# Optimization experiments

Measured on AMD Instinct MI355X. Metric: run time of the kernel, lower is better.

The kernel has to match this reference:

```python
import jax, jax.numpy as jnp
import numpy as np

B, S, D = 4, 2048, 2048
H = 16
Q_LORA = 1536
KV_LORA = 512
D_NOPE = 128
D_ROPE = 64
D_V = 128
MLP = 8192
EPS = 1e-6
THETA = 10000.0


def rmsnorm(x, scale, eps=EPS):
    var = jnp.mean(jnp.square(x.astype(jnp.float32)), axis=-1, keepdims=True)
    return (x * jax.lax.rsqrt(var + eps)).astype(x.dtype) * scale


def rope(x, positions):
    # x: [B, S, H, d], positions: [B, S]
    d = x.shape[-1]
    inv_freq = 1.0 / (THETA ** (jnp.arange(0, d, 2, dtype=jnp.float32) / d))
    ang = positions.astype(jnp.float32)[..., None] * inv_freq  # [B,S,d/2]
    cos = jnp.cos(ang)[:, :, None, :]
    sin = jnp.sin(ang)[:, :, None, :]
    x1, x2 = jnp.split(x, 2, axis=-1)
    return jnp.concatenate([x1 * cos - x2 * sin, x2 * cos + x1 * sin], axis=-1)


def setup_inputs() -> dict:
    key = jax.random.key(0)
    ks = jax.random.split(key, 16)
    sd = lambda fan: 1.0 / np.sqrt(fan)
    inp = {
        'inputs': jax.random.normal(ks[0], (B, S, D), jnp.float32),
        'decoder_segment_ids': jnp.ones((B, S), jnp.int32),
        'decoder_positions': jnp.broadcast_to(jnp.arange(S, dtype=jnp.int32), (B, S)),
        'pre_ln_scale': jnp.ones((D,), jnp.float32),
        'post_ln_scale': jnp.ones((D,), jnp.float32),
        'q_ln_scale': jnp.ones((Q_LORA,), jnp.float32),
        'kv_ln_scale': jnp.ones((KV_LORA,), jnp.float32),
        'wq_a': jax.random.normal(ks[1], (D, Q_LORA), jnp.float32) * sd(D),
        'wq_b': jax.random.normal(ks[2], (Q_LORA, H, D_NOPE + D_ROPE), jnp.float32) * sd(Q_LORA),
        'wkv_a': jax.random.normal(ks[3], (D, KV_LORA + D_ROPE), jnp.float32) * sd(D),
        'wkv_b': jax.random.normal(ks[4], (KV_LORA, H, D_NOPE + D_V), jnp.float32) * sd(KV_LORA),
        'wo_attn': jax.random.normal(ks[5], (H, D_V, D), jnp.float32) * sd(H * D_V),
        'wi_0': jax.random.normal(ks[6], (D, MLP), jnp.float32) * sd(D),
        'wi_1': jax.random.normal(ks[7], (D, MLP), jnp.float32) * sd(D),
        'wo_mlp': jax.random.normal(ks[8], (MLP, D), jnp.float32) * sd(MLP),
    }
    return inp


def reference(inputs, decoder_segment_ids, decoder_positions, pre_ln_scale, post_ln_scale,
              q_ln_scale, kv_ln_scale, wq_a, wq_b, wkv_a, wkv_b, wo_attn, wi_0, wi_1, wo_mlp):
    # ---- pre-norm ----
    lnx = rmsnorm(inputs, pre_ln_scale)

    # ---- MLA attention ----
    # low-rank query: down-proj, norm, up-proj
    q_c = rmsnorm(lnx @ wq_a, q_ln_scale)                       # [B,S,Q_LORA]
    q = jnp.einsum('bsr,rhd->bshd', q_c, wq_b)                  # [B,S,H,nope+rope]
    q_nope, q_rope = q[..., :D_NOPE], q[..., D_NOPE:]

    # compressed kv + decoupled rope key
    kv = lnx @ wkv_a                                            # [B,S,KV_LORA+rope]
    c_kv = rmsnorm(kv[..., :KV_LORA], kv_ln_scale)
    k_rope = kv[..., KV_LORA:][:, :, None, :]                   # [B,S,1,rope]
    kvu = jnp.einsum('bsr,rhd->bshd', c_kv, wkv_b)              # [B,S,H,nope+v]
    k_nope, v = kvu[..., :D_NOPE], kvu[..., D_NOPE:]

    q_rope = rope(q_rope, decoder_positions)
    k_rope = rope(k_rope, decoder_positions)
    k_rope = jnp.broadcast_to(k_rope, (B, S, H, D_ROPE))

    qf = jnp.concatenate([q_nope, q_rope], axis=-1)             # [B,S,H,192]
    kf = jnp.concatenate([k_nope, k_rope], axis=-1)

    scale = 1.0 / np.sqrt(D_NOPE + D_ROPE)
    scores = jnp.einsum('bqhd,bkhd->bhqk', qf, kf) * scale      # [B,H,S,S]

    pos = decoder_positions
    seg = decoder_segment_ids
    mask = (pos[:, :, None] >= pos[:, None, :]) & (seg[:, :, None] == seg[:, None, :])
    scores = jnp.where(mask[:, None, :, :], scores, -1e9)
    probs = jax.nn.softmax(scores, axis=-1)

    attn = jnp.einsum('bhqk,bkhd->bqhd', probs, v)              # [B,S,H,D_V]
    attn_out = jnp.einsum('bqhd,hdm->bqm', attn, wo_attn)       # [B,S,D]

    # ---- residual + post-norm ----
    intermediate = inputs + attn_out
    hidden = rmsnorm(intermediate, post_ln_scale)

    # ---- gated MLP (silu * linear) ----
    mlp = (jax.nn.silu(hidden @ wi_0) * (hidden @ wi_1)) @ wo_mlp

    return mlp + intermediate
```

## Files before the change

kernel.cpp:

```cpp
#include <hip/hip_runtime.h>
#include <stdint.h>

typedef unsigned short u16;
typedef __bf16 bf16x8 __attribute__((ext_vector_type(8)));
typedef float f32x4 __attribute__((ext_vector_type(4)));

#define B_ 4
#define S_ 2048
#define H_ 16
#define TOK (B_*S_)
#define MFMA_B16 __builtin_amdgcn_mfma_f32_16x16x32_bf16

__device__ __forceinline__ u16 f32_bf16(float f) {
    union { float f; unsigned int u; } x; x.f = f;
    return (u16)((x.u + 0x7fffu + ((x.u >> 16) & 1u)) >> 16);
}
__device__ __forceinline__ float bf2f(u16 v) {
    union { unsigned int u; float f; } x; x.u = ((unsigned int)v) << 16; return x.f;
}
__device__ __forceinline__ void gld_lds16(const u16* g, u16* lds) {
    __builtin_amdgcn_global_load_lds(
        (const __attribute__((address_space(1))) unsigned int*)g,
        (__attribute__((address_space(3))) unsigned int*)lds, 16, 0, 0);
}

__global__ void fill_sentinel(float* o, int n) {
    int i = blockIdx.x * 256 + threadIdx.x;
    if (i < n) o[i] = 12345.0f;
}

__global__ __launch_bounds__(256) void transpose_f32_bf16(const float* __restrict__ in, u16* __restrict__ out,
                                                          int K, int N, int Npad) {
    __shared__ float t[32][33];
    int nb = blockIdx.x * 32, kb = blockIdx.y * 32;
    int c = threadIdx.x & 31, r = threadIdx.x >> 5;
#pragma unroll
    for (int i = 0; i < 4; ++i) {
        int kk = kb + r + i * 8, nn = nb + c;
        t[r + i * 8][c] = (kk < K && nn < N) ? in[(size_t)kk * N + nn] : 0.f;
    }
    __syncthreads();
#pragma unroll
    for (int i = 0; i < 4; ++i) {
        int no = nb + r + i * 8, ko = kb + c;
        if (no < Npad && ko < K) out[(size_t)no * K + ko] = f32_bf16(t[c][r + i * 8]);
    }
}

__global__ __launch_bounds__(256) void rmsnorm_f32(const float* __restrict__ in, const float* __restrict__ sc,
                                                   u16* __restrict__ out, int N) {
    int row = blockIdx.x;
    const float* x = in + (size_t)row * N;
    float ss = 0.f;
    for (int c = threadIdx.x * 4; c < N; c += 1024) {
        float4 v = *(const float4*)(x + c);
        ss += v.x * v.x + v.y * v.y + v.z * v.z + v.w * v.w;
    }
#pragma unroll
    for (int off = 32; off; off >>= 1) ss += __shfl_down(ss, off);
    __shared__ float red[4];
    if ((threadIdx.x & 63) == 0) red[threadIdx.x >> 6] = ss;
    __syncthreads();
    float rs = rsqrtf((red[0] + red[1] + red[2] + red[3]) / (float)N + 1e-6f);
    for (int c = threadIdx.x * 4; c < N; c += 1024) {
        float4 v = *(const float4*)(x + c);
        float4 s4 = *(const float4*)(sc + c);
        ushort4 ov;
        ov.x = f32_bf16(v.x * rs * s4.x);
        ov.y = f32_bf16(v.y * rs * s4.y);
        ov.z = f32_bf16(v.z * rs * s4.z);
        ov.w = f32_bf16(v.w * rs * s4.w);
        *(ushort4*)&out[(size_t)row * N + c] = ov;
    }
}

__global__ __launch_bounds__(256) void rmsnorm_bf16(const u16* __restrict__ in, const float* __restrict__ sc,
                                                    u16* __restrict__ out, int N) {
    int row = blockIdx.x;
    const u16* x = in + (size_t)row * N;
    float ss = 0.f;
    for (int c = threadIdx.x * 8; c < N; c += 2048) {
        ushort4 v0 = *(const ushort4*)(x + c);
        ushort4 v1 = *(const ushort4*)(x + c + 4);
        float f0 = bf2f(v0.x), f1 = bf2f(v0.y), f2 = bf2f(v0.z), f3 = bf2f(v0.w);
        float f4 = bf2f(v1.x), f5 = bf2f(v1.y), f6 = bf2f(v1.z), f7 = bf2f(v1.w);
        ss += f0*f0 + f1*f1 + f2*f2 + f3*f3 + f4*f4 + f5*f5 + f6*f6 + f7*f7;
    }
#pragma unroll
    for (int off = 32; off; off >>= 1) ss += __shfl_down(ss, off);
    __shared__ float red[4];
    if ((threadIdx.x & 63) == 0) red[threadIdx.x >> 6] = ss;
    __syncthreads();
    float rs = rsqrtf((red[0] + red[1] + red[2] + red[3]) / (float)N + 1e-6f);
    for (int c = threadIdx.x * 8; c < N; c += 2048) {
        ushort4 v0 = *(const ushort4*)(x + c);
        ushort4 v1 = *(const ushort4*)(x + c + 4);
        ushort4 o0, o1;
        o0.x = f32_bf16(bf2f(v0.x) * rs * sc[c + 0]);
        o0.y = f32_bf16(bf2f(v0.y) * rs * sc[c + 1]);
        o0.z = f32_bf16(bf2f(v0.z) * rs * sc[c + 2]);
        o0.w = f32_bf16(bf2f(v0.w) * rs * sc[c + 3]);
        o1.x = f32_bf16(bf2f(v1.x) * rs * sc[c + 4]);
        o1.y = f32_bf16(bf2f(v1.y) * rs * sc[c + 5]);
        o1.z = f32_bf16(bf2f(v1.z) * rs * sc[c + 6]);
        o1.w = f32_bf16(bf2f(v1.w) * rs * sc[c + 7]);
        *(ushort4*)&out[(size_t)row * N + c] = o0;
        *(ushort4*)&out[(size_t)row * N + c + 4] = o1;
    }
}

__global__ __launch_bounds__(128) void kv_post(const u16* __restrict__ kv, const float* __restrict__ scale,
                                               const int* __restrict__ pos, u16* __restrict__ ckv,
                                               u16* __restrict__ kr) {
    int row = blockIdx.x;
    const u16* x = kv + (size_t)row * 640;
    int c = threadIdx.x * 4;
    ushort4 v = *(const ushort4*)(x + c);
    float f0 = bf2f(v.x), f1 = bf2f(v.y), f2 = bf2f(v.z), f3 = bf2f(v.w);
    float ss = f0*f0 + f1*f1 + f2*f2 + f3*f3;
#pragma unroll
    for (int off = 32; off; off >>= 1) ss += __shfl_down(ss, off);
    __shared__ float red[2];
    if ((threadIdx.x & 63) == 0) red[threadIdx.x >> 6] = ss;
    __syncthreads();
    float rs = rsqrtf((red[0] + red[1]) * (1.f / 512.f) + 1e-6f);
    float4 s4 = *(const float4*)(scale + c);
    ushort4 ov;
    ov.x = f32_bf16(f0 * rs * s4.x);
    ov.y = f32_bf16(f1 * rs * s4.y);
    ov.z = f32_bf16(f2 * rs * s4.z);
    ov.w = f32_bf16(f3 * rs * s4.w);
    *(ushort4*)&ckv[(size_t)row * 512 + c] = ov;
    if (threadIdx.x < 32) {
        int i = threadIdx.x;
        float x1 = bf2f(x[512 + i]), x2 = bf2f(x[544 + i]);
        float inv = expf(-(float)(2 * i) * (1.f / 64.f) * 9.2103403719761836f);
        float ang = (float)pos[row] * inv;
        float sn, cs; sincosf(ang, &sn, &cs);
        kr[(size_t)row * 64 + i]      = f32_bf16(x1 * cs - x2 * sn);
        kr[(size_t)row * 64 + 32 + i] = f32_bf16(x2 * cs + x1 * sn);
    }
}

__global__ __launch_bounds__(64) void q_rope_inplace(u16* __restrict__ q, const int* __restrict__ pos) {
    int token = blockIdx.x, h = blockIdx.y;
    u16* p = q + ((size_t)token * 16 + h) * 192;
    int t = threadIdx.x, i = t & 31;
    float x1 = bf2f(p[128 + i]), x2 = bf2f(p[160 + i]);
    float inv = expf(-(float)(2 * i) * (1.f / 64.f) * 9.2103403719761836f);
    float ang = (float)pos[token] * inv;
    float sn, cs; sincosf(ang, &sn, &cs);
    float val = (t < 32) ? (x1 * cs - x2 * sn) : (x2 * cs + x1 * sn);
    p[128 + t] = f32_bf16(val);
}

__global__ __launch_bounds__(320) void kv_build(const u16* __restrict__ kvu, const u16* __restrict__ kr,
                                                u16* __restrict__ kf, u16* __restrict__ vf, int tok0) {
    int local = blockIdx.x, h = blockIdx.y;
    int token = tok0 + local;
    int b = token >> 11, s = token & 2047;
    int bh = b * 16 + h;
    int tile = s >> 6, ki = s & 63;
    const u16* u = kvu + ((size_t)local * 16 + h) * 256;
    int t = threadIdx.x;
    if (t < 192) {
        u16 val = (t < 128) ? u[t] : kr[(size_t)token * 64 + (t - 128)];
        int byte = (ki * 384 + t * 2) ^ ((ki & 7) << 4);
        kf[(size_t)bh * (S_ * 192) + (size_t)tile * 12288 + (byte >> 1)] = val;
    } else {
        int dv = t - 192;
        u16 val = u[128 + dv];
        int byte = (dv * 128 + ki * 2) ^ ((dv & 7) << 4);
        vf[(size_t)bh * (S_ * 128) + (size_t)tile * 8192 + (byte >> 1)] = val;
    }
}

__global__ __launch_bounds__(256) void gemm128(const u16* __restrict__ A, const u16* __restrict__ Bt,
                                               u16* __restrict__ C, int M, int N, int K) {
    __shared__ u16 As[128 * 32];
    __shared__ u16 Bs[128 * 32];
    const int l = threadIdx.x & 63, w = threadIdx.x >> 6;
    const int wr = w >> 1, wc = w & 1;
    const int m0 = blockIdx.y * 128, n0 = blockIdx.x * 128;
    const int lm = l & 15, lg = l >> 4;
    const int srow = l >> 2, sk = (l & 3) * 8;
    f32x4 acc[4][4] = {};
    for (int k0 = 0; k0 < K; k0 += 32) {
#pragma unroll
        for (int i = 0; i < 2; ++i) {
            int c = w * 2 + i;
            gld_lds16(A  + (size_t)(m0 + c * 16 + srow) * K + k0 + sk, &As[c * 512]);
            gld_lds16(Bt + (size_t)(n0 + c * 16 + srow) * K + k0 + sk, &Bs[c * 512]);
        }
        __syncthreads();
        bf16x8 a[4], b[4];
#pragma unroll
        for (int m = 0; m < 4; ++m) a[m] = *(const bf16x8*)&As[(wr * 64 + m * 16 + lm) * 32 + lg * 8];
#pragma unroll
        for (int n = 0; n < 4; ++n) b[n] = *(const bf16x8*)&Bs[(wc * 64 + n * 16 + lm) * 32 + lg * 8];
#pragma unroll
        for (int m = 0; m < 4; ++m)
#pragma unroll
            for (int n = 0; n < 4; ++n)
                acc[m][n] = MFMA_B16(a[m], b[n], acc[m][n], 0, 0, 0);
        __syncthreads();
    }
#pragma unroll
    for (int m = 0; m < 4; ++m)
#pragma unroll
        for (int j = 0; j < 4; ++j) {
            int row = m0 + wr * 64 + m * 16 + lg * 4 + j;
            size_t base = (size_t)row * N + n0 + wc * 64;
#pragma unroll
            for (int n = 0; n < 4; ++n)
                C[base + n * 16 + lm] = f32_bf16(acc[m][n][j]);
        }
}

template<int EPI>
__global__ __launch_bounds__(512, 2) void gemm256(const u16* __restrict__ A, const u16* __restrict__ Bt,
                                                  void* __restrict__ Cv, const void* __restrict__ Rv,
                                                  int M, int N, int K) {
    __shared__ u16 lds[65536];
    char* ldsb = (char*)lds;
    const int tid = threadIdx.x;
    const int l = tid & 63, w = tid >> 6;
    const int wr = w >> 2, wcn = w & 3;
    const int lm = l & 15, lg = l >> 4;
    const int m0 = blockIdx.y * 256, n0 = blockIdx.x * 256;

    int srow[2], scb[2];
#pragma unroll
    for (int ld = 0; ld < 2; ++ld) {
        int P = tid * 16 + ld * 8192;
        int L = P ^ (((P >> 7) & 7) << 4);
        srow[ld] = L >> 7; scb[ld] = L & 127;
    }
    const u16* Ablk = A + (size_t)m0 * K;
    const u16* Bblk = Bt + (size_t)n0 * K;

    f32x4 acc[8][4] = {};

    auto stage = [&](const u16* gp, int h, int kt, int db, int streamoff) {
#pragma unroll
        for (int ld = 0; ld < 2; ++ld) {
            const u16* src = gp + (size_t)(h * 128 + srow[ld]) * K + kt * 64 + (scb[ld] >> 1);
            u16* dst = (u16*)(ldsb + db * 65536 + streamoff + h * 16384 + w * 1024 + ld * 8192);
            gld_lds16(src, dst);
        }
    };
    auto readA = [&](int db, int fm, int ks) -> bf16x8 {
        int row = wr * 128 + fm * 16 + lm;
        int cb = lg * 16 + ks * 64;
        return *(const bf16x8*)(ldsb + db * 65536 + row * 128 + (cb ^ ((row & 7) << 4)));
    };
    auto readB = [&](int db, int fn, int ks) -> bf16x8 {
        int row = wcn * 64 + fn * 16 + lm;
        int cb = lg * 16 + ks * 64;
        return *(const bf16x8*)(ldsb + db * 65536 + 32768 + row * 128 + (cb ^ ((row & 7) << 4)));
    };

    const int ntile = K >> 6;
#pragma unroll
    for (int h = 0; h < 2; ++h) stage(Ablk, h, 0, 0, 0);
#pragma unroll
    for (int h = 0; h < 2; ++h) stage(Bblk, h, 0, 0, 32768);
    asm volatile("s_waitcnt vmcnt(0)" ::: "memory");
    __builtin_amdgcn_s_barrier();

    for (int t = 0; t < ntile; ++t) {
        const int db = t & 1;
        bf16x8 bfr[4][2];
        bf16x8 a0 = readA(db, 0, 0), a1 = readA(db, 0, 1);
        bf16x8 a2 = readA(db, 1, 0), a3 = readA(db, 1, 1);
#pragma unroll
        for (int fn = 0; fn < 4; ++fn) { bfr[fn][0] = readB(db, fn, 0); bfr[fn][1] = readB(db, fn, 1); }
        if (t + 1 < ntile) {
#pragma unroll
            for (int h = 0; h < 2; ++h) stage(Ablk, h, t + 1, db ^ 1, 0);
#pragma unroll
            for (int h = 0; h < 2; ++h) stage(Bblk, h, t + 1, db ^ 1, 32768);
        }
        __builtin_amdgcn_s_barrier();
        asm volatile("s_waitcnt lgkmcnt(0)" ::: "memory");
        __builtin_amdgcn_sched_barrier(0);
        __builtin_amdgcn_s_setprio(1);
#pragma unroll
        for (int fn = 0; fn < 4; ++fn) {
            acc[0][fn] = MFMA_B16(a0, bfr[fn][0], acc[0][fn], 0, 0, 0);
            acc[0][fn] = MFMA_B16(a1, bfr[fn][1], acc[0][fn], 0, 0, 0);
            acc[1][fn] = MFMA_B16(a2, bfr[fn][0], acc[1][fn], 0, 0, 0);
            acc[1][fn] = MFMA_B16(a3, bfr[fn][1], acc[1][fn], 0, 0, 0);
        }
        __builtin_amdgcn_s_setprio(0);
        __builtin_amdgcn_s_barrier();
#pragma unroll
        for (int p = 1; p < 4; ++p) {
            a0 = readA(db, 2 * p, 0);     a1 = readA(db, 2 * p, 1);
            a2 = readA(db, 2 * p + 1, 0); a3 = readA(db, 2 * p + 1, 1);
            if (p == 3) asm volatile("s_waitcnt vmcnt(0)" ::: "memory");
            __builtin_amdgcn_s_barrier();
            asm volatile("s_waitcnt lgkmcnt(0)" ::: "memory");
            __builtin_amdgcn_sched_barrier(0);
            __builtin_amdgcn_s_setprio(1);
#pragma unroll
            for (int fn = 0; fn < 4; ++fn) {
                acc[2*p][fn]   = MFMA_B16(a0, bfr[fn][0], acc[2*p][fn], 0, 0, 0);
                acc[2*p][fn]   = MFMA_B16(a1, bfr[fn][1], acc[2*p][fn], 0, 0, 0);
                acc[2*p+1][fn] = MFMA_B16(a2, bfr[fn][0], acc[2*p+1][fn], 0, 0, 0);
                acc[2*p+1][fn] = MFMA_B16(a3, bfr[fn][1], acc[2*p+1][fn], 0, 0, 0);
            }
            __builtin_amdgcn_s_setprio(0);
            __builtin_amdgcn_s_barrier();
        }
    }
#pragma unroll
    for (int fm = 0; fm < 8; ++fm)
#pragma unroll
        for (int j = 0; j < 4; ++j) {
            int row = m0 + wr * 128 + fm * 16 + lg * 4 + j;
            size_t base = (size_t)row * N + n0 + wcn * 64;
#pragma unroll
            for (int fn = 0; fn < 4; ++fn) {
                size_t idx = base + fn * 16 + lm;
                float v = acc[fm][fn][j];
                if (EPI == 0) {
                    ((u16*)Cv)[idx] = f32_bf16(v);
                } else if (EPI == 1) {
                    ((float*)Cv)[idx] = v + ((const float*)Rv)[idx];
                } else {
                    float x0 = bf2f(((const u16*)Rv)[idx]);
                    float sl = x0 / (1.f + expf(-x0));
                    ((u16*)Cv)[idx] = f32_bf16(sl * v);
                }
            }
        }
}

__global__ __launch_bounds__(256) void attn_fwd(const u16* __restrict__ qf, const u16* __restrict__ kfs,
                                                const u16* __restrict__ vfs, u16* __restrict__ attn) {
    __shared__ u16 Ks[64 * 192];
    __shared__ u16 Vs[128 * 64];
    __shared__ u16 Ps[4][1024];
    const int px = blockIdx.x;
    const int bh = blockIdx.y;
    const int b = bh >> 4, h = bh & 15;
    const int l = threadIdx.x & 63, w = threadIdx.x >> 6;
    const int lm = l & 15, g = l >> 4;
    const u16* kb0 = kfs + (size_t)bh * (S_ * 192);
    const u16* vb0 = vfs + (size_t)bh * (S_ * 128);
    const float scale = 0.07216878364870322f;

    for (int pass = 0; pass < 2; ++pass) {
        const int qb = pass ? (31 - px) : px;
        const int qrow = qb * 64 + w * 16 + lm;
        const u16* qp = qf + (((size_t)(b * S_ + qrow)) * 16 + h) * 192 + g * 8;
        bf16x8 qr[6];
#pragma unroll
        for (int c = 0; c < 6; ++c) qr[c] = *(const bf16x8*)(qp + c * 32);
        f32x4 o[8] = {};
        float mrow[4] = {-1e30f, -1e30f, -1e30f, -1e30f};
        float lrow[4] = {0.f, 0.f, 0.f, 0.f};
        for (int kt = 0; kt <= qb; ++kt) {
            const u16* kc = kb0 + (size_t)kt * 12288;
            const u16* vc = vb0 + (size_t)kt * 8192;
#pragma unroll
            for (int i = 0; i < 6; ++i) {
                int c = w + i * 4;
                gld_lds16(kc + c * 512 + l * 8, &Ks[c * 512]);
            }
#pragma unroll
            for (int i = 0; i < 4; ++i) {
                int c = w + i * 4;
                gld_lds16(vc + c * 512 + l * 8, &Vs[c * 512]);
            }
            __syncthreads();
            f32x4 sc[4] = {};
#pragma unroll
            for (int nf = 0; nf < 4; ++nf) {
                int key = nf * 16 + lm;
                int kswz = (key & 7) << 4;
#pragma unroll
                for (int c = 0; c < 6; ++c) {
                    int byte = (key * 384 + (c * 32 + g * 8) * 2) ^ kswz;
                    bf16x8 kv = *(const bf16x8*)((const char*)Ks + byte);
                    sc[nf] = MFMA_B16(qr[c], kv, sc[nf], 0, 0, 0);
                }
            }
#pragma unroll
            for (int j = 0; j < 4; ++j) {
                const int q_g = qb * 64 + w * 16 + g * 4 + j;
                float mx = -1e30f;
#pragma unroll
                for (int nf = 0; nf < 4; ++nf) {
                    int key_g = kt * 64 + nf * 16 + lm;
                    float v = sc[nf][j] * scale;
                    v = (key_g > q_g) ? -1e30f : v;
                    sc[nf][j] = v;
                    mx = fmaxf(mx, v);
                }
                mx = fmaxf(mx, __shfl_xor(mx, 1));
                mx = fmaxf(mx, __shfl_xor(mx, 2));
                mx = fmaxf(mx, __shfl_xor(mx, 4));
                mx = fmaxf(mx, __shfl_xor(mx, 8));
                float newm = fmaxf(mrow[j], mx);
                float fac = __expf(mrow[j] - newm);
                mrow[j] = newm;
                float rs = 0.f;
                u16 pb[4];
#pragma unroll
                for (int nf = 0; nf < 4; ++nf) {
                    float pv = __expf(sc[nf][j] - newm);
                    rs += pv;
                    pb[nf] = f32_bf16(pv);
                }
                rs += __shfl_xor(rs, 1);
                rs += __shfl_xor(rs, 2);
                rs += __shfl_xor(rs, 4);
                rs += __shfl_xor(rs, 8);
                lrow[j] = lrow[j] * fac + rs;
#pragma unroll
                for (int n = 0; n < 8; ++n) o[n][j] *= fac;
                int row = g * 4 + j;
                int rswz = (row & 7) << 4;
#pragma unroll
                for (int nf = 0; nf < 4; ++nf) {
                    int byte = (row * 128 + (nf * 16 + lm) * 2) ^ rswz;
                    *(u16*)((char*)&Ps[w][0] + byte) = pb[nf];
                }
            }
#pragma unroll
            for (int kc2 = 0; kc2 < 2; ++kc2) {
                int pbyte = (lm * 128 + (kc2 * 32 + g * 8) * 2) ^ ((lm & 7) << 4);
                bf16x8 pa = *(const bf16x8*)((const char*)&Ps[w][0] + pbyte);
#pragma unroll
                for (int n = 0; n < 8; ++n) {
                    int dv = n * 16 + lm;
                    int vbyte = (dv * 128 + (kc2 * 32 + g * 8) * 2) ^ ((dv & 7) << 4);
                    bf16x8 vv = *(const bf16x8*)((const char*)Vs + vbyte);
                    o[n] = MFMA_B16(pa, vv, o[n], 0, 0, 0);
                }
            }
            __syncthreads();
        }
#pragma unroll
        for (int j = 0; j < 4; ++j) {
            float inv = 1.f / lrow[j];
            int s = qb * 64 + w * 16 + g * 4 + j;
            size_t base = ((size_t)(b * S_ + s)) * (H_ * 128) + h * 128;
#pragma unroll
            for (int n = 0; n < 8; ++n)
                attn[base + n * 16 + lm] = f32_bf16(o[n][j] * inv);
        }
    }
}

extern "C" void kernel_launch(void* const* d_in, const int* in_sizes, int n_in,
                              void* d_out, int out_size, void* d_ws, size_t ws_size,
                              hipStream_t stream) {
    (void)in_sizes; (void)n_in;
    const float* inputs = (const float*)d_in[0];
    const int*   pos    = (const int*)d_in[2];
    const float* pre_s  = (const float*)d_in[3];
    const float* post_s = (const float*)d_in[4];
    const float* q_s    = (const float*)d_in[5];
    const float* kv_s   = (const float*)d_in[6];
    const float* wq_a   = (const float*)d_in[7];
    const float* wq_b   = (const float*)d_in[8];
    const float* wkv_a  = (const float*)d_in[9];
    const float* wkv_b  = (const float*)d_in[10];
    const float* wo_at  = (const float*)d_in[11];
    const float* wi0    = (const float*)d_in[12];
    const float* wi1    = (const float*)d_in[13];
    const float* wom    = (const float*)d_in[14];
    float* out = (float*)d_out;

    char* p = (char*)d_ws;
    auto alloc = [&](size_t n) { char* r = p; p += (n + 255) & ~(size_t)255; return r; };
    char* R1   = alloc((size_t)134217728);
    u16* vf    = (u16*)alloc((size_t)33554432);
    u16* aslot = (u16*)alloc((size_t)33554432);
    u16* wslot = (u16*)alloc((size_t)33554432);
    u16* ckv   = (u16*)alloc((size_t)8388608);
    u16* krope = (u16*)alloc((size_t)1048576);
    if ((size_t)(p - (char*)d_ws) > ws_size) {
        fill_sentinel<<<(out_size + 255) / 256, 256, 0, stream>>>(out, out_size);
        return;
    }
    u16* kf    = (u16*)R1;
    u16* q_c   = (u16*)R1;
    u16* kvtmp = (u16*)(R1 + 25165824);
    u16* q     = (u16*)(R1 + 50331648);
    u16* lnx   = (u16*)(R1 + 100663296);
    u16* kvu   = (u16*)(R1 + 100663296);
    u16* X     = (u16*)R1;

    rmsnorm_f32<<<TOK, 256, 0, stream>>>(inputs, pre_s, lnx, 2048);
    transpose_f32_bf16<<<dim3(48, 64), 256, 0, stream>>>(wq_a, wslot, 2048, 1536, 1536);
    gemm256<0><<<dim3(6, 32), 512, 0, stream>>>(lnx, wslot, q_c, nullptr, TOK, 1536, 2048);
    rmsnorm_bf16<<<TOK, 256, 0, stream>>>(q_c, q_s, q_c, 1536);
    transpose_f32_bf16<<<dim3(20, 64), 256, 0, stream>>>(wkv_a, wslot, 2048, 576, 640);
    gemm128<<<dim3(5, 64), 256, 0, stream>>>(lnx, wslot, kvtmp, TOK, 640, 2048);
    kv_post<<<TOK, 128, 0, stream>>>(kvtmp, kv_s, pos, ckv, krope);
    transpose_f32_bf16<<<dim3(96, 48), 256, 0, stream>>>(wq_b, wslot, 1536, 3072, 3072);
    gemm256<0><<<dim3(12, 32), 512, 0, stream>>>(q_c, wslot, q, nullptr, TOK, 3072, 1536);
    q_rope_inplace<<<dim3(TOK, 16), 64, 0, stream>>>(q, pos);
    transpose_f32_bf16<<<dim3(128, 16), 256, 0, stream>>>(wkv_b, wslot, 512, 4096, 4096);
    for (int ch = 0; ch < 2; ++ch) {
        int t0 = ch * 4096;
        gemm256<0><<<dim3(16, 16), 512, 0, stream>>>(ckv + (size_t)t0 * 512, wslot, kvu, nullptr, 4096, 4096, 512);
        kv_build<<<dim3(4096, 16), 320, 0, stream>>>(kvu, krope, kf, vf, t0);
    }
    attn_fwd<<<dim3(16, 64), 256, 0, stream>>>(q, kf, vf, aslot);
    transpose_f32_bf16<<<dim3(64, 64), 256, 0, stream>>>(wo_at, wslot, 2048, 2048, 2048);
    gemm256<1><<<dim3(8, 32), 512, 0, stream>>>(aslot, wslot, out, inputs, TOK, 2048, 2048);
    rmsnorm_f32<<<TOK, 256, 0, stream>>>(out, post_s, aslot, 2048);
    transpose_f32_bf16<<<dim3(256, 64), 256, 0, stream>>>(wi0, wslot, 2048, 8192, 8192);
    gemm256<0><<<dim3(32, 32), 512, 0, stream>>>(aslot, wslot, X, nullptr, TOK, 8192, 2048);
    transpose_f32_bf16<<<dim3(256, 64), 256, 0, stream>>>(wi1, wslot, 2048, 8192, 8192);
    gemm256<2><<<dim3(32, 32), 512, 0, stream>>>(aslot, wslot, X, X, TOK, 8192, 2048);
    transpose_f32_bf16<<<dim3(64, 256), 256, 0, stream>>>(wom, wslot, 8192, 2048, 2048);
    gemm256<1><<<dim3(8, 32), 512, 0, stream>>>(X, wslot, out, out, TOK, 2048, 8192);
}
```

Before: 1.652 ms.

## Restructure gemm256 main loop into 4-stage K=32 pipeline with split A/B prefetch

```diff
diff --git a/kernel.cpp b/kernel.cpp
--- a/kernel.cpp
+++ b/kernel.cpp
@@ -229,90 +229,105 @@
     const int lm = l & 15, lg = l >> 4;
     const int m0 = blockIdx.y * 256, n0 = blockIdx.x * 256;
 
-    int srow[2], scb[2];
+    int gm[2], gk[2];
 #pragma unroll
     for (int ld = 0; ld < 2; ++ld) {
         int P = tid * 16 + ld * 8192;
-        int L = P ^ (((P >> 7) & 7) << 4);
-        srow[ld] = L >> 7; scb[ld] = L & 127;
-    }
-    const u16* Ablk = A + (size_t)m0 * K;
-    const u16* Bblk = Bt + (size_t)n0 * K;
+        int row = P >> 7;
+        int un = (P & 127) ^ ((row & 7) << 4);
+        gm[ld] = row * 2 + (un >> 6);
+        gk[ld] = (un & 63) >> 1;
+    }
+    const u16* Ab = A + (size_t)m0 * K;
+    const u16* Bb = Bt + (size_t)n0 * K;
 
     f32x4 acc[8][4] = {};
 
-    auto stage = [&](const u16* gp, int h, int kt, int db, int streamoff) {
-#pragma unroll
-        for (int ld = 0; ld < 2; ++ld) {
-            const u16* src = gp + (size_t)(h * 128 + srow[ld]) * K + kt * 64 + (scb[ld] >> 1);
-            u16* dst = (u16*)(ldsb + db * 65536 + streamoff + h * 16384 + w * 1024 + ld * 8192);
-            gld_lds16(src, dst);
-        }
+    auto stageA = [&](int t) {
+#pragma unroll
+        for (int ld = 0; ld < 2; ++ld)
+            gld_lds16(Ab + (size_t)gm[ld] * K + t * 32 + gk[ld],
+                      (u16*)(ldsb + (t & 3) * 32768 + tid * 16 + ld * 8192));
     };
-    auto readA = [&](int db, int fm, int ks) -> bf16x8 {
-        int row = wr * 128 + fm * 16 + lm;
-        int cb = lg * 16 + ks * 64;
-        return *(const bf16x8*)(ldsb + db * 65536 + row * 128 + (cb ^ ((row & 7) << 4)));
+    auto stageB = [&](int t) {
+#pragma unroll
+        for (int ld = 0; ld < 2; ++ld)
+            gld_lds16(Bb + (size_t)gm[ld] * K + t * 32 + gk[ld],
+                      (u16*)(ldsb + (t & 3) * 32768 + 16384 + tid * 16 + ld * 8192));
     };
-    auto readB = [&](int db, int fn, int ks) -> bf16x8 {
-        int row = wcn * 64 + fn * 16 + lm;
-        int cb = lg * 16 + ks * 64;
-        return *(const bf16x8*)(ldsb + db * 65536 + 32768 + row * 128 + (cb ^ ((row & 7) << 4)));
+    auto readA = [&](int buf, int fm) -> bf16x8 {
+        int m = wr * 128 + fm * 16 + lm;
+        int off = ((m & 1) * 64 + lg * 16) ^ (((m >> 1) & 7) << 4);
+        return *(const bf16x8*)(ldsb + buf * 32768 + (m >> 1) * 128 + off);
     };
-
-    const int ntile = K >> 6;
-#pragma unroll
-    for (int h = 0; h < 2; ++h) stage(Ablk, h, 0, 0, 0);
-#pragma unroll
-    for (int h = 0; h < 2; ++h) stage(Bblk, h, 0, 0, 32768);
-    asm volatile("s_waitcnt vmcnt(0)" ::: "memory");
+    auto readB = [&](int buf, int fn) -> bf16x8 {
+        int n = wcn * 64 + fn * 16 + lm;
+        int off = ((n & 1) * 64 + lg * 16) ^ (((n >> 1) & 7) << 4);
+        return *(const bf16x8*)(ldsb + buf * 32768 + 16384 + (n >> 1) * 128 + off);
+    };
+
+    const int ntile = K >> 5;
+    stageA(0); stageB(0);
+    stageA(1); stageB(1);
+    stageA(2); stageB(2);
+    asm volatile("s_waitcnt vmcnt(8)" ::: "memory");
     __builtin_amdgcn_s_barrier();
 
+#pragma unroll 1
     for (int t = 0; t < ntile; ++t) {
-        const int db = t & 1;
-        bf16x8 bfr[4][2];
-        bf16x8 a0 = readA(db, 0, 0), a1 = readA(db, 0, 1);
-        bf16x8 a2 = readA(db, 1, 0), a3 = readA(db, 1, 1);
-#pragma unroll
-        for (int fn = 0; fn < 4; ++fn) { bfr[fn][0] = readB(db, fn, 0); bfr[fn][1] = readB(db, fn, 1); }
-        if (t + 1 < ntile) {
-#pragma unroll
-            for (int h = 0; h < 2; ++h) stage(Ablk, h, t + 1, db ^ 1, 0);
-#pragma unroll
-            for (int h = 0; h < 2; ++h) stage(Bblk, h, t + 1, db ^ 1, 32768);
-        }
+        const int buf = t & 3;
+        bf16x8 b0 = readB(buf, 0), b1 = readB(buf, 1), b2 = readB(buf, 2), b3 = readB(buf, 3);
+        bf16x8 a0 = readA(buf, 0), a1 = readA(buf, 1), a2 = readA(buf, 2), a3 = readA(buf, 3);
+        if (t + 3 < ntile) stageA(t + 3);
+        asm volatile("s_waitcnt lgkmcnt(0)" ::: "memory");
         __builtin_amdgcn_s_barrier();
-        asm volatile("s_waitcnt lgkmcnt(0)" ::: "memory");
         __builtin_amdgcn_sched_barrier(0);
         __builtin_amdgcn_s_setprio(1);
-#pragma unroll
-        for (int fn = 0; fn < 4; ++fn) {
-            acc[0][fn] = MFMA_B16(a0, bfr[fn][0], acc[0][fn], 0, 0, 0);
-            acc[0][fn] = MFMA_B16(a1, bfr[fn][1], acc[0][fn], 0, 0, 0);
-            acc[1][fn] = MFMA_B16(a2, bfr[fn][0], acc[1][fn], 0, 0, 0);
-            acc[1][fn] = MFMA_B16(a3, bfr[fn][1], acc[1][fn], 0, 0, 0);
-        }
+        acc[0][0] = MFMA_B16(a0, b0, acc[0][0], 0, 0, 0);
+        acc[0][1] = MFMA_B16(a0, b1, acc[0][1], 0, 0, 0);
+        acc[0][2] = MFMA_B16(a0, b2, acc[0][2], 0, 0, 0);
+        acc[0][3] = MFMA_B16(a0, b3, acc[0][3], 0, 0, 0);
+        acc[1][0] = MFMA_B16(a1, b0, acc[1][0], 0, 0, 0);
+        acc[1][1] = MFMA_B16(a1, b1, acc[1][1], 0, 0, 0);
+        acc[1][2] = MFMA_B16(a1, b2, acc[1][2], 0, 0, 0);
+        acc[1][3] = MFMA_B16(a1, b3, acc[1][3], 0, 0, 0);
+        acc[2][0] = MFMA_B16(a2, b0, acc[2][0], 0, 0, 0);
+        acc[2][1] = MFMA_B16(a2, b1, acc[2][1], 0, 0, 0);
+        acc[2][2] = MFMA_B16(a2, b2, acc[2][2], 0, 0, 0);
+        acc[2][3] = MFMA_B16(a2, b3, acc[2][3], 0, 0, 0);
+        acc[3][0] = MFMA_B16(a3, b0, acc[3][0], 0, 0, 0);
+        acc[3][1] = MFMA_B16(a3, b1, acc[3][1], 0, 0, 0);
+        acc[3][2] = MFMA_B16(a3, b2, acc[3][2], 0, 0, 0);
+        acc[3][3] = MFMA_B16(a3, b3, acc[3][3], 0, 0, 0);
         __builtin_amdgcn_s_setprio(0);
         __builtin_amdgcn_s_barrier();
-#pragma unroll
-        for (int p = 1; p < 4; ++p) {
-            a0 = readA(db, 2 * p, 0);     a1 = readA(db, 2 * p, 1);
-            a2 = readA(db, 2 * p + 1, 0); a3 = readA(db, 2 * p + 1, 1);
-            if (p == 3) asm volatile("s_waitcnt vmcnt(0)" ::: "memory");
-            __builtin_amdgcn_s_barrier();
-            asm volatile("s_waitcnt lgkmcnt(0)" ::: "memory");
-            __builtin_amdgcn_sched_barrier(0);
-            __builtin_amdgcn_s_setprio(1);
-#pragma unroll
-            for (int fn = 0; fn < 4; ++fn) {
-                acc[2*p][fn]   = MFMA_B16(a0, bfr[fn][0], acc[2*p][fn], 0, 0, 0);
-                acc[2*p][fn]   = MFMA_B16(a1, bfr[fn][1], acc[2*p][fn], 0, 0, 0);
-                acc[2*p+1][fn] = MFMA_B16(a2, bfr[fn][0], acc[2*p+1][fn], 0, 0, 0);
-                acc[2*p+1][fn] = MFMA_B16(a3, bfr[fn][1], acc[2*p+1][fn], 0, 0, 0);
-            }
-            __builtin_amdgcn_s_setprio(0);
-            __builtin_amdgcn_s_barrier();
-        }
+        a0 = readA(buf, 4); a1 = readA(buf, 5); a2 = readA(buf, 6); a3 = readA(buf, 7);
+        if (t + 3 < ntile) stageB(t + 3);
+        asm volatile("s_waitcnt lgkmcnt(0)" ::: "memory");
+        if (t < ntile - 3)       { asm volatile("s_waitcnt vmcnt(8)" ::: "memory"); }
+        else if (t == ntile - 3) { asm volatile("s_waitcnt vmcnt(4)" ::: "memory"); }
+        else if (t == ntile - 2) { asm volatile("s_waitcnt vmcnt(0)" ::: "memory"); }
+        __builtin_amdgcn_s_barrier();
+        __builtin_amdgcn_sched_barrier(0);
+        __builtin_amdgcn_s_setprio(1);
+        acc[4][0] = MFMA_B16(a0, b0, acc[4][0], 0, 0, 0);
+        acc[4][1] = MFMA_B16(a0, b1, acc[4][1], 0, 0, 0);
+        acc[4][2] = MFMA_B16(a0, b2, acc[4][2], 0, 0, 0);
+        acc[4][3] = MFMA_B16(a0, b3, acc[4][3], 0, 0, 0);
+        acc[5][0] = MFMA_B16(a1, b0, acc[5][0], 0, 0, 0);
+        acc[5][1] = MFMA_B16(a1, b1, acc[5][1], 0, 0, 0);
+        acc[5][2] = MFMA_B16(a1, b2, acc[5][2], 0, 0, 0);
+        acc[5][3] = MFMA_B16(a1, b3, acc[5][3], 0, 0, 0);
+        acc[6][0] = MFMA_B16(a2, b0, acc[6][0], 0, 0, 0);
+        acc[6][1] = MFMA_B16(a2, b1, acc[6][1], 0, 0, 0);
+        acc[6][2] = MFMA_B16(a2, b2, acc[6][2], 0, 0, 0);
+        acc[6][3] = MFMA_B16(a2, b3, acc[6][3], 0, 0, 0);
+        acc[7][0] = MFMA_B16(a3, b0, acc[7][0], 0, 0, 0);
+        acc[7][1] = MFMA_B16(a3, b1, acc[7][1], 0, 0, 0);
+        acc[7][2] = MFMA_B16(a3, b2, acc[7][2], 0, 0, 0);
+        acc[7][3] = MFMA_B16(a3, b3, acc[7][3], 0, 0, 0);
+        __builtin_amdgcn_s_setprio(0);
+        __builtin_amdgcn_s_barrier();
     }
 #pragma unroll
     for (int fm = 0; fm < 8; ++fm)
```

Result: slower. 1.736 ms (+5.1%).
